# Kernel optimization log

Measured on AMD Instinct MI355X. Metric: run time of the kernel, lower is better.

Reference implementation:

```python
import jax, jax.numpy as jnp
import numpy as np


def cv_sigmoid(z):
    # split sigmoid: sigmoid(Re) + i*sigmoid(Im)
    return jax.nn.sigmoid(z.real) + 1j * jax.nn.sigmoid(z.imag)


def cv_polar_tanh(z):
    # tanh on magnitude, phase preserved: tanh(|z|) * z / |z|
    mag = jnp.abs(z)
    safe = jnp.where(mag == 0, 1.0, mag)
    return (jnp.tanh(mag) / safe).astype(z.dtype) * z


def setup_inputs() -> dict:
    key = jax.random.key(0)
    B, D, H = 16384, 512, 512
    ks = jax.random.split(key, 12)
    names = ['x_re', 'x_im', 'h_re', 'h_im', 'Wx_re', 'Wx_im', 'Wh_re', 'Wh_im', 'bx_re', 'bx_im', 'bh_re', 'bh_im']
    shapes = [(B, D), (B, D), (B, H), (B, H), (3, H, D), (3, H, D), (3, H, H), (3, H, H), (3, H), (3, H), (3, H), (3, H)]
    out = {}
    for n, s, k in zip(names, shapes, ks):
        scale = 1.0 if n[0] in ('x', 'h') else (1.0 / np.sqrt(s[-1]))
        out[n] = jax.random.normal(k, s, dtype=jnp.float32) * scale
    return out


def reference(x_re, x_im, h_re, h_im, Wx_re, Wx_im, Wh_re, Wh_im, bx_re, bx_im, bh_re, bh_im):
    x = (x_re + 1j * x_im).astype(jnp.complex64)   # [B, D]
    h = (h_re + 1j * h_im).astype(jnp.complex64)   # [B, H]
    Wx = (Wx_re + 1j * Wx_im).astype(jnp.complex64)  # [3, H, D] (z, r, h)
    Wh = (Wh_re + 1j * Wh_im).astype(jnp.complex64)  # [3, H, H]
    bx = (bx_re + 1j * bx_im).astype(jnp.complex64)  # [3, H]
    bh = (bh_re + 1j * bh_im).astype(jnp.complex64)  # [3, H]

    # input projections for all three gates at once: [3, B, H]
    px = jnp.einsum('bd,khd->kbh', x, Wx) + bx[:, None, :]
    # hidden projections for z and r gates
    pz = jnp.einsum('bh,gh->bg', h, Wh[0]) + bh[0]
    pr = jnp.einsum('bh,gh->bg', h, Wh[1]) + bh[1]

    z = cv_sigmoid(px[0] + pz)
    r = cv_sigmoid(px[1] + pr)

    ph = jnp.einsum('bh,gh->bg', r * h, Wh[2]) + bh[2]
    h_tilde = cv_polar_tanh(px[2] + ph)

    h_new = (1.0 - z) * h + z * h_tilde  # [B, H] complex
    # return as stacked real/imag float tensor [B, H, 2]
    return jnp.stack([h_new.real, h_new.imag], axis=-1)
```

## Files before the change

### kernel.cpp

```cpp
#include <hip/hip_runtime.h>
#include <hip/hip_bf16.h>

typedef __bf16 bf16_t;
typedef __bf16 bf16x8 __attribute__((ext_vector_type(8)));
typedef __bf16 bf16x4 __attribute__((ext_vector_type(4)));
typedef float f32x4 __attribute__((ext_vector_type(4)));


__device__ __forceinline__ void gl_lds16(const bf16_t* g, bf16_t* l) {
  __builtin_amdgcn_global_load_lds(
      (const __attribute__((address_space(1))) void*)g,
      (__attribute__((address_space(3))) void*)l, 16, 0, 0);
}

__device__ __forceinline__ float fast_sigmoid(float x) {
  return 1.0f / (1.0f + __expf(-x));
}

__global__ void pack_A(const float* __restrict__ x_re, const float* __restrict__ x_im,
                       const float* __restrict__ h_re, const float* __restrict__ h_im,
                       bf16_t* __restrict__ A) {
  int q = blockIdx.x * blockDim.x + threadIdx.x;
  int i4 = q << 2;
  int b = i4 >> 11;
  int k = i4 & 2047;
  int seg = k >> 9;
  int off = k & 511;
  const float* s = (seg == 0) ? x_re : (seg == 1) ? x_im : (seg == 2) ? h_re : h_im;
  const float4 v = *(const float4*)(s + (size_t)b * 512 + off);
  bf16x4 o = { (bf16_t)v.x, (bf16_t)v.y, (bf16_t)v.z, (bf16_t)v.w };
  *(bf16x4*)(A + (size_t)b * 2048 + k) = o;
}

__global__ void pack_W(const float* __restrict__ Wx_re, const float* __restrict__ Wx_im,
                       const float* __restrict__ Wh_re, const float* __restrict__ Wh_im,
                       bf16_t* __restrict__ W1t, bf16_t* __restrict__ W2t) {
  int q = blockIdx.x * blockDim.x + threadIdx.x;
  int n, k2, g, j, p;
  const float *Wre, *Wim;
  bf16_t* dst;
  if (q < 1048576) {
    n = q >> 9; k2 = (q & 511) << 2;
    g = n >> 10; j = (n & 1023) >> 1; p = n & 1;
    int pair = k2 >> 10;
    Wre = pair ? Wh_re : Wx_re;
    Wim = pair ? Wh_im : Wx_im;
    dst = W1t + (size_t)n * 2048 + k2;
  } else if (q < 1048576 + 262144) {
    int q2 = q - 1048576;
    n = 2048 + (q2 >> 8); k2 = (q2 & 255) << 2;
    g = 2; j = (n - 2048) >> 1; p = n & 1;
    Wre = Wx_re; Wim = Wx_im;
    dst = W1t + (size_t)n * 2048 + k2;
  } else {
    int q3 = q - (1048576 + 262144);
    n = q3 >> 8; k2 = (q3 & 255) << 2;
    g = 2; j = n >> 1; p = n & 1;
    Wre = Wh_re; Wim = Wh_im;
    dst = W2t + (size_t)n * 1024 + k2;
  }
  int klocal = k2 & 1023;
  int half = klocal >> 9;
  int off = klocal & 511;
  size_t sidx = ((size_t)g * 512 + j) * 512 + off;
  const float* s = (half == 0) ? (p ? Wim : Wre) : (p ? Wre : Wim);
  float sgn = (half == 1 && p == 0) ? -1.0f : 1.0f;
  float4 v = *(const float4*)(s + sidx);
  bf16x4 o = { (bf16_t)(sgn * v.x), (bf16_t)(sgn * v.y),
               (bf16_t)(sgn * v.z), (bf16_t)(sgn * v.w) };
  *(bf16x4*)dst = o;
}

template <int MODE>
__launch_bounds__(512, 2)
__global__ void gemm_fused(const bf16_t* __restrict__ A, const bf16_t* __restrict__ W,
                           int LDA, int LDW,
                           bf16_t* __restrict__ zbuf, bf16_t* __restrict__ A2,
                           float* __restrict__ outbuf,
                           const float* __restrict__ h_re, const float* __restrict__ h_im,
                           const float* __restrict__ bx_re, const float* __restrict__ bx_im,
                           const float* __restrict__ bh_re, const float* __restrict__ bh_im) {
  __shared__ __align__(16) bf16_t As[2][256 * 64];
  __shared__ __align__(16) bf16_t Bs[2][256 * 64];

  const int bid = blockIdx.x;
  const int xcd = bid & 7;
  const int idx = bid >> 3;
  const int ntile = idx >> 3;
  const int mtile = (xcd << 3) + (idx & 7);
  const int m0 = mtile * 256;
  const int n0 = ntile * 256;
  const int region = (MODE == 1) ? (ntile >> 2) : 0;
  const int KEND = (MODE == 1) ? ((region < 2) ? 2048 : 1024) : 1024;
  const int nKT = KEND >> 6;

  const int tid = threadIdx.x;
  const int lane = tid & 63;
  const int w = tid >> 6;
  const int wr = w >> 2;
  const int wc = w & 3;

  const int rb = tid >> 3;
  const int cc = tid & 7;
  const int cs = cc ^ (rb & 7);
  const bf16_t* Ag = A + (size_t)(m0 + rb) * LDA + cs * 8;
  const bf16_t* Wg = W + (size_t)(n0 + rb) * LDW + cs * 8;

#define STAGE_A(s, bufi, kt2) \
  gl_lds16(Ag + (size_t)(s) * 64 * LDA + (kt2) * 64, &As[bufi][tid * 8 + (s) * 4096])
#define STAGE_B(s, bufi, kt2) \
  gl_lds16(Wg + (size_t)(s) * 64 * LDW + (kt2) * 64, &Bs[bufi][tid * 8 + (s) * 4096])

  const int quad = lane >> 4, lrow = lane & 15;
  int aOff[8], bOff[4];
#pragma unroll
  for (int mt = 0; mt < 8; ++mt) {
    const int r = wr * 128 + mt * 16 + lrow;
    aOff[mt] = r * 64 + ((quad ^ (r & 7)) << 3);
  }
#pragma unroll
  for (int nt = 0; nt < 4; ++nt) {
    const int r = wc * 64 + nt * 16 + lrow;
    bOff[nt] = r * 64 + ((quad ^ (r & 7)) << 3);
  }

  f32x4 acc[8][4] = {};

#pragma unroll
  for (int s = 0; s < 4; ++s) STAGE_A(s, 0, 0);
#pragma unroll
  for (int s = 0; s < 4; ++s) STAGE_B(s, 0, 0);
  STAGE_A(0, 1, 1);
  STAGE_A(2, 1, 1);
  asm volatile("s_waitcnt vmcnt(2)" ::: "memory");
  __builtin_amdgcn_s_barrier();

  for (int kt = 0; kt < nKT; ++kt) {
    const int b = kt & 1;
    const bf16_t* Ab = As[b];
    const bf16_t* Bb = Bs[b];
    const bool s1 = (kt + 1 < nKT);
    const bool s2 = (kt + 2 < nKT);

    bf16x8 bk0[4], bk1[4], aA[4], aB[4], aC[4], aD[4];

#pragma unroll
    for (int nt = 0; nt < 4; ++nt) bk0[nt] = *(const bf16x8*)(Bb + bOff[nt]);
#pragma unroll
    for (int i = 0; i < 4; ++i) aA[i] = *(const bf16x8*)(Ab + aOff[i]);
#pragma unroll
    for (int i = 0; i < 4; ++i) aB[i] = *(const bf16x8*)(Ab + aOff[4 + i]);
    if (s1) { STAGE_A(1, b ^ 1, kt + 1); STAGE_A(3, b ^ 1, kt + 1); }
    __builtin_amdgcn_s_setprio(1);
#pragma unroll
    for (int i = 0; i < 4; ++i)
#pragma unroll
      for (int nt = 0; nt < 4; ++nt)
        acc[i][nt] = __builtin_amdgcn_mfma_f32_16x16x32_bf16(aA[i], bk0[nt], acc[i][nt], 0, 0, 0);
    __builtin_amdgcn_s_setprio(0);

#pragma unroll
    for (int i = 0; i < 4; ++i) aC[i] = *(const bf16x8*)(Ab + (aOff[i] ^ 32));
#pragma unroll
    for (int nt = 0; nt < 4; ++nt) bk1[nt] = *(const bf16x8*)(Bb + (bOff[nt] ^ 32));
    if (s1) { STAGE_B(0, b ^ 1, kt + 1); STAGE_B(1, b ^ 1, kt + 1); }
    __builtin_amdgcn_s_setprio(1);
#pragma unroll
    for (int i = 0; i < 4; ++i)
#pragma unroll
      for (int nt = 0; nt < 4; ++nt)
        acc[4 + i][nt] = __builtin_amdgcn_mfma_f32_16x16x32_bf16(aB[i], bk0[nt], acc[4 + i][nt], 0, 0, 0);
    __builtin_amdgcn_s_setprio(0);

#pragma unroll
    for (int i = 0; i < 4; ++i) aD[i] = *(const bf16x8*)(Ab + (aOff[4 + i] ^ 32));
    if (s1) { STAGE_B(2, b ^ 1, kt + 1); STAGE_B(3, b ^ 1, kt + 1); }
    __builtin_amdgcn_s_setprio(1);
#pragma unroll
    for (int i = 0; i < 4; ++i)
#pragma unroll
      for (int nt = 0; nt < 4; ++nt)
        acc[i][nt] = __builtin_amdgcn_mfma_f32_16x16x32_bf16(aC[i], bk1[nt], acc[i][nt], 0, 0, 0);
    __builtin_amdgcn_s_setprio(0);

    asm volatile("" ::: "memory");
    __builtin_amdgcn_s_barrier();

    if (s2) { STAGE_A(0, b, kt + 2); STAGE_A(2, b, kt + 2); }
    __builtin_amdgcn_s_setprio(1);
#pragma unroll
    for (int i = 0; i < 4; ++i)
#pragma unroll
      for (int nt = 0; nt < 4; ++nt)
        acc[4 + i][nt] = __builtin_amdgcn_mfma_f32_16x16x32_bf16(aD[i], bk1[nt], acc[4 + i][nt], 0, 0, 0);
    __builtin_amdgcn_s_setprio(0);

    if (s1) {
      if (s2) asm volatile("s_waitcnt vmcnt(2)" ::: "memory");
      else    asm volatile("s_waitcnt vmcnt(0)" ::: "memory");
      asm volatile("" ::: "memory");
      __builtin_amdgcn_s_barrier();
    }
  }
#undef STAGE_A
#undef STAGE_B

#pragma unroll
  for (int mt = 0; mt < 8; ++mt) {
#pragma unroll
    for (int nt = 0; nt < 4; ++nt) {
#pragma unroll
      for (int rg = 0; rg < 4; ++rg) {
        const int m = m0 + wr * 128 + mt * 16 + quad * 4 + rg;
        const int n = n0 + wc * 64 + nt * 16 + lrow;
        float v = acc[mt][nt][rg];
        const int p = n & 1;

        if (MODE == 1) {
          const int cj = n & 1023;
          const int j = cj >> 1;
          const float bias = p ? (bx_im[region * 512 + j] + bh_im[region * 512 + j])
                               : (bx_re[region * 512 + j] + bh_re[region * 512 + j]);
          const float val = v + bias;
          if (region == 0) {
            zbuf[(size_t)m * 1024 + cj] = (bf16_t)fast_sigmoid(val);
          } else if (region == 1) {
            float rv = fast_sigmoid(val);
            float ro = __shfl_xor(rv, 1, 64);
            float hp = p ? h_im[(size_t)m * 512 + j] : h_re[(size_t)m * 512 + j];
            float ho = __shfl_xor(hp, 1, 64);
            float rh = (p == 0) ? (rv * hp - ro * ho) : (ro * hp + rv * ho);
            A2[(size_t)m * 1024 + p * 512 + j] = (bf16_t)rh;
          } else {
            outbuf[(size_t)m * 1024 + cj] = val;
          }
        } else {
          const int j = n >> 1;
          float tv = outbuf[(size_t)m * 1024 + n];
          float u = tv + v;
          float uo = __shfl_xor(u, 1, 64);
          float mag = sqrtf(u * u + uo * uo);
          float mm = fminf(mag, 20.0f);
          float e = __expf(2.0f * mm);
          float th = (e - 1.0f) / (e + 1.0f);
          float s = (mag == 0.0f) ? 0.0f : (th / mag);
          float hto = s * u;
          float htd = s * uo;
          float zv = (float)zbuf[(size_t)m * 1024 + n];
          float zo = __shfl_xor(zv, 1, 64);
          float hp = p ? h_im[(size_t)m * 512 + j] : h_re[(size_t)m * 512 + j];
          float ho = __shfl_xor(hp, 1, 64);
          float res;
          if (p == 0)
            res = (1.0f - zv) * hp + zo * ho + zv * hto - zo * htd;
          else
            res = (1.0f - zo) * hp - zv * ho + zo * hto + zv * htd;
          outbuf[(size_t)m * 1024 + n] = res;
        }
      }
    }
  }
}

extern "C" void kernel_launch(void* const* d_in, const int* in_sizes, int n_in,
                              void* d_out, int out_size, void* d_ws, size_t ws_size,
                              hipStream_t stream) {
  const float* x_re  = (const float*)d_in[0];
  const float* x_im  = (const float*)d_in[1];
  const float* h_re  = (const float*)d_in[2];
  const float* h_im  = (const float*)d_in[3];
  const float* Wx_re = (const float*)d_in[4];
  const float* Wx_im = (const float*)d_in[5];
  const float* Wh_re = (const float*)d_in[6];
  const float* Wh_im = (const float*)d_in[7];
  const float* bx_re = (const float*)d_in[8];
  const float* bx_im = (const float*)d_in[9];
  const float* bh_re = (const float*)d_in[10];
  const float* bh_im = (const float*)d_in[11];
  float* out = (float*)d_out;

  char* ws = (char*)d_ws;
  bf16_t* A_big = (bf16_t*)(ws);
  bf16_t* W1t   = (bf16_t*)(ws + 67108864);
  bf16_t* W2t   = (bf16_t*)(ws + 79691776);
  bf16_t* A2    = (bf16_t*)(ws + 81788928);
  bf16_t* zbuf  = (bf16_t*)(ws + 115343360);

  pack_A<<<32768, 256, 0, stream>>>(x_re, x_im, h_re, h_im, A_big);
  pack_W<<<6144, 256, 0, stream>>>(Wx_re, Wx_im, Wh_re, Wh_im, W1t, W2t);
  gemm_fused<1><<<768, 512, 0, stream>>>(A_big, W1t, 2048, 2048,
      zbuf, A2, out, h_re, h_im, bx_re, bx_im, bh_re, bh_im);
  gemm_fused<2><<<256, 512, 0, stream>>>(A2, W2t, 1024, 1024,
      zbuf, A2, out, h_re, h_im, bx_re, bx_im, bh_re, bh_im);
}
```

Measured before the change: 629.3 us.

## Shrink GEMM tiles to 128x128 with 256-thread blocks and simpler pipeline

Both fused GEMM kernels now use 128x128 output tiles computed by four waves instead of 256x256 tiles with eight waves. The grids grow to 3072 and 1024 blocks with a new XCD-aware tile mapping. The staggered prefetch schedule is replaced by a plain double buffer that loads the whole next K-tile and then does a full vmcnt(0) wait and barrier. Smaller tiles give more blocks per CU and better load balance, but each loaded byte is reused less, global and L2 traffic rises, and the simpler pipeline hides less memory latency.

```diff
diff --git a/kernel.cpp b/kernel.cpp
--- a/kernel.cpp
+++ b/kernel.cpp
@@ -72,7 +72,7 @@
 }
 
 template <int MODE>
-__launch_bounds__(512, 2)
+__launch_bounds__(256, 2)
 __global__ void gemm_fused(const bf16_t* __restrict__ A, const bf16_t* __restrict__ W,
                            int LDA, int LDW,
                            bf16_t* __restrict__ zbuf, bf16_t* __restrict__ A2,
@@ -80,25 +80,26 @@
                            const float* __restrict__ h_re, const float* __restrict__ h_im,
                            const float* __restrict__ bx_re, const float* __restrict__ bx_im,
                            const float* __restrict__ bh_re, const float* __restrict__ bh_im) {
-  __shared__ __align__(16) bf16_t As[2][256 * 64];
-  __shared__ __align__(16) bf16_t Bs[2][256 * 64];
+  __shared__ __align__(16) bf16_t As[2][128 * 64];
+  __shared__ __align__(16) bf16_t Bs[2][128 * 64];
 
   const int bid = blockIdx.x;
   const int xcd = bid & 7;
   const int idx = bid >> 3;
-  const int ntile = idx >> 3;
-  const int mtile = (xcd << 3) + (idx & 7);
-  const int m0 = mtile * 256;
-  const int n0 = ntile * 256;
-  const int region = (MODE == 1) ? (ntile >> 2) : 0;
+  const int NT = (MODE == 1) ? 24 : 8;
+  const int ntile = idx % NT;
+  const int mtile = (xcd << 4) + idx / NT;
+  const int m0 = mtile * 128;
+  const int n0 = ntile * 128;
+  const int region = (MODE == 1) ? (ntile >> 3) : 0;
   const int KEND = (MODE == 1) ? ((region < 2) ? 2048 : 1024) : 1024;
   const int nKT = KEND >> 6;
 
   const int tid = threadIdx.x;
   const int lane = tid & 63;
   const int w = tid >> 6;
-  const int wr = w >> 2;
-  const int wc = w & 3;
+  const int wr = w >> 1;
+  const int wc = w & 1;
 
   const int rb = tid >> 3;
   const int cc = tid & 7;
@@ -107,15 +108,15 @@
   const bf16_t* Wg = W + (size_t)(n0 + rb) * LDW + cs * 8;
 
 #define STAGE_A(s, bufi, kt2) \
-  gl_lds16(Ag + (size_t)(s) * 64 * LDA + (kt2) * 64, &As[bufi][tid * 8 + (s) * 4096])
+  gl_lds16(Ag + (size_t)(s) * 32 * LDA + (kt2) * 64, &As[bufi][tid * 8 + (s) * 2048])
 #define STAGE_B(s, bufi, kt2) \
-  gl_lds16(Wg + (size_t)(s) * 64 * LDW + (kt2) * 64, &Bs[bufi][tid * 8 + (s) * 4096])
+  gl_lds16(Wg + (size_t)(s) * 32 * LDW + (kt2) * 64, &Bs[bufi][tid * 8 + (s) * 2048])
 
   const int quad = lane >> 4, lrow = lane & 15;
-  int aOff[8], bOff[4];
-#pragma unroll
-  for (int mt = 0; mt < 8; ++mt) {
-    const int r = wr * 128 + mt * 16 + lrow;
+  int aOff[4], bOff[4];
+#pragma unroll
+  for (int mt = 0; mt < 4; ++mt) {
+    const int r = wr * 64 + mt * 16 + lrow;
     aOff[mt] = r * 64 + ((quad ^ (r & 7)) << 3);
   }
 #pragma unroll
@@ -124,15 +125,13 @@
     bOff[nt] = r * 64 + ((quad ^ (r & 7)) << 3);
   }
 
-  f32x4 acc[8][4] = {};
-
+  f32x4 acc[4][4] = {};
+
+#pragma unroll
+  for (int s = 0; s < 4; ++s) STAGE_B(s, 0, 0);
 #pragma unroll
   for (int s = 0; s < 4; ++s) STAGE_A(s, 0, 0);
-#pragma unroll
-  for (int s = 0; s < 4; ++s) STAGE_B(s, 0, 0);
-  STAGE_A(0, 1, 1);
-  STAGE_A(2, 1, 1);
-  asm volatile("s_waitcnt vmcnt(2)" ::: "memory");
+  asm volatile("s_waitcnt vmcnt(0)" ::: "memory");
   __builtin_amdgcn_s_barrier();
 
   for (int kt = 0; kt < nKT; ++kt) {
@@ -140,78 +139,52 @@
     const bf16_t* Ab = As[b];
     const bf16_t* Bb = Bs[b];
     const bool s1 = (kt + 1 < nKT);
-    const bool s2 = (kt + 2 < nKT);
-
-    bf16x8 bk0[4], bk1[4], aA[4], aB[4], aC[4], aD[4];
-
-#pragma unroll
-    for (int nt = 0; nt < 4; ++nt) bk0[nt] = *(const bf16x8*)(Bb + bOff[nt]);
-#pragma unroll
-    for (int i = 0; i < 4; ++i) aA[i] = *(const bf16x8*)(Ab + aOff[i]);
-#pragma unroll
-    for (int i = 0; i < 4; ++i) aB[i] = *(const bf16x8*)(Ab + aOff[4 + i]);
-    if (s1) { STAGE_A(1, b ^ 1, kt + 1); STAGE_A(3, b ^ 1, kt + 1); }
+
+    bf16x8 ak[4], bk[4];
+
+#pragma unroll
+    for (int i = 0; i < 4; ++i) bk[i] = *(const bf16x8*)(Bb + bOff[i]);
+#pragma unroll
+    for (int i = 0; i < 4; ++i) ak[i] = *(const bf16x8*)(Ab + aOff[i]);
+    if (s1) {
+#pragma unroll
+      for (int s = 0; s < 4; ++s) STAGE_B(s, b ^ 1, kt + 1);
+#pragma unroll
+      for (int s = 0; s < 4; ++s) STAGE_A(s, b ^ 1, kt + 1);
+    }
     __builtin_amdgcn_s_setprio(1);
 #pragma unroll
     for (int i = 0; i < 4; ++i)
 #pragma unroll
-      for (int nt = 0; nt < 4; ++nt)
-        acc[i][nt] = __builtin_amdgcn_mfma_f32_16x16x32_bf16(aA[i], bk0[nt], acc[i][nt], 0, 0, 0);
+      for (int j2 = 0; j2 < 4; ++j2)
+        acc[i][j2] = __builtin_amdgcn_mfma_f32_16x16x32_bf16(ak[i], bk[j2], acc[i][j2], 0, 0, 0);
     __builtin_amdgcn_s_setprio(0);
 
 #pragma unroll
-    for (int i = 0; i < 4; ++i) aC[i] = *(const bf16x8*)(Ab + (aOff[i] ^ 32));
-#pragma unroll
-    for (int nt = 0; nt < 4; ++nt) bk1[nt] = *(const bf16x8*)(Bb + (bOff[nt] ^ 32));
-    if (s1) { STAGE_B(0, b ^ 1, kt + 1); STAGE_B(1, b ^ 1, kt + 1); }
+    for (int i = 0; i < 4; ++i) bk[i] = *(const bf16x8*)(Bb + (bOff[i] ^ 32));
+#pragma unroll
+    for (int i = 0; i < 4; ++i) ak[i] = *(const bf16x8*)(Ab + (aOff[i] ^ 32));
     __builtin_amdgcn_s_setprio(1);
 #pragma unroll
     for (int i = 0; i < 4; ++i)
 #pragma unroll
-      for (int nt = 0; nt < 4; ++nt)
-        acc[4 + i][nt] = __builtin_amdgcn_mfma_f32_16x16x32_bf16(aB[i], bk0[nt], acc[4 + i][nt], 0, 0, 0);
+      for (int j2 = 0; j2 < 4; ++j2)
+        acc[i][j2] = __builtin_amdgcn_mfma_f32_16x16x32_bf16(ak[i], bk[j2], acc[i][j2], 0, 0, 0);
     __builtin_amdgcn_s_setprio(0);
 
-#pragma unroll
-    for (int i = 0; i < 4; ++i) aD[i] = *(const bf16x8*)(Ab + (aOff[4 + i] ^ 32));
-    if (s1) { STAGE_B(2, b ^ 1, kt + 1); STAGE_B(3, b ^ 1, kt + 1); }
-    __builtin_amdgcn_s_setprio(1);
-#pragma unroll
-    for (int i = 0; i < 4; ++i)
-#pragma unroll
-      for (int nt = 0; nt < 4; ++nt)
-        acc[i][nt] = __builtin_amdgcn_mfma_f32_16x16x32_bf16(aC[i], bk1[nt], acc[i][nt], 0, 0, 0);
-    __builtin_amdgcn_s_setprio(0);
-
-    asm volatile("" ::: "memory");
+    if (s1) asm volatile("s_waitcnt vmcnt(0)" ::: "memory");
     __builtin_amdgcn_s_barrier();
-
-    if (s2) { STAGE_A(0, b, kt + 2); STAGE_A(2, b, kt + 2); }
-    __builtin_amdgcn_s_setprio(1);
-#pragma unroll
-    for (int i = 0; i < 4; ++i)
-#pragma unroll
-      for (int nt = 0; nt < 4; ++nt)
-        acc[4 + i][nt] = __builtin_amdgcn_mfma_f32_16x16x32_bf16(aD[i], bk1[nt], acc[4 + i][nt], 0, 0, 0);
-    __builtin_amdgcn_s_setprio(0);
-
-    if (s1) {
-      if (s2) asm volatile("s_waitcnt vmcnt(2)" ::: "memory");
-      else    asm volatile("s_waitcnt vmcnt(0)" ::: "memory");
-      asm volatile("" ::: "memory");
-      __builtin_amdgcn_s_barrier();
-    }
   }
 #undef STAGE_A
 #undef STAGE_B
 
 #pragma unroll
-  for (int mt = 0; mt < 8; ++mt) {
+  for (int mt = 0; mt < 4; ++mt) {
 #pragma unroll
     for (int nt = 0; nt < 4; ++nt) {
 #pragma unroll
       for (int rg = 0; rg < 4; ++rg) {
-        const int m = m0 + wr * 128 + mt * 16 + quad * 4 + rg;
+        const int m = m0 + wr * 64 + mt * 16 + quad * 4 + rg;
         const int n = n0 + wc * 64 + nt * 16 + lrow;
         float v = acc[mt][nt][rg];
         const int p = n & 1;
@@ -288,8 +261,8 @@
 
   pack_A<<<32768, 256, 0, stream>>>(x_re, x_im, h_re, h_im, A_big);
   pack_W<<<6144, 256, 0, stream>>>(Wx_re, Wx_im, Wh_re, Wh_im, W1t, W2t);
-  gemm_fused<1><<<768, 512, 0, stream>>>(A_big, W1t, 2048, 2048,
+  gemm_fused<1><<<3072, 256, 0, stream>>>(A_big, W1t, 2048, 2048,
       zbuf, A2, out, h_re, h_im, bx_re, bx_im, bh_re, bh_im);
-  gemm_fused<2><<<256, 512, 0, stream>>>(A2, W2t, 1024, 1024,
+  gemm_fused<2><<<1024, 256, 0, stream>>>(A2, W2t, 1024, 1024,
       zbuf, A2, out, h_re, h_im, bx_re, bx_im, bh_re, bh_im);
 }
```

Result: slower. 753.4 us (+19.7%).
